# Kernel tuning notes

Hardware: AMD Instinct MI355X
Metric: run time of the kernel (lower is better)

Reference implementation:

```python
import jax, jax.numpy as jnp
import numpy as np

INPUT_SIZE = 64
HIDDEN = 128
BATCH = 256
SEQ = 2048


def setup_inputs() -> dict:
    key = jax.random.key(0)
    k_x, k_w, k_r = jax.random.split(key, 3)
    x = jax.random.normal(k_x, (BATCH, SEQ, INPUT_SIZE), dtype=jnp.float32)
    # Gate order: i, f, o, z (stacked). W: (4H, I), R: (H, 4H), b: (4H,)
    W = jax.random.normal(k_w, (4 * HIDDEN, INPUT_SIZE), dtype=jnp.float32) * (1.0 / np.sqrt(INPUT_SIZE))
    R = jax.random.normal(k_r, (HIDDEN, 4 * HIDDEN), dtype=jnp.float32) * (1.0 / np.sqrt(HIDDEN))
    b = jnp.zeros((4 * HIDDEN,), dtype=jnp.float32)
    return {"x": x, "W": W, "R": R, "b": b}


def _slstm_scan(x, W, R, b):
    B, S, _ = x.shape
    H = R.shape[0]
    # Precompute input projections for all timesteps: (B, S, 4H)
    pre = jnp.einsum('bsi,gi->bsg', x, W) + b
    pre = jnp.swapaxes(pre, 0, 1)  # (S, B, 4H)

    def step(carry, pre_t):
        h, c, n, m = carry
        gates = pre_t + h @ R  # (B, 4H); note: matmul(h, r), NOT r.T (as in source)
        i_t, f_t, o_t, z_t = jnp.split(gates, 4, axis=-1)
        # log(exp(i_tilda)) == i_tilda; log(sigmoid(f_tilda)) stabilized
        log_f = jax.nn.log_sigmoid(f_t)
        m_new = jnp.maximum(log_f + m, i_t)
        i_p = jnp.exp(i_t - m_new)
        f_p = jnp.exp(log_f + m - m_new)
        c_new = f_p * c + i_p * jnp.tanh(z_t)
        n_new = f_p * n + i_p
        h_new = jax.nn.sigmoid(o_t) * jnp.tanh(c_new / n_new)
        return (h_new, c_new, n_new, m_new), h_new

    z = jnp.zeros((B, H), dtype=x.dtype)
    (_h, _c, _n, _m), hs = jax.lax.scan(step, (z, z, z, z), pre)
    return jnp.swapaxes(hs, 0, 1)  # (B, S, H)


def reference(x, W, R, b):
    return _slstm_scan(x, W, R, b)
```

## Files before the change

### kernel.cpp

```cpp
#include <hip/hip_runtime.h>
#include <hip/hip_fp16.h>

#define BATCH 256
#define SEQ   2048
#define ISZ   64
#define HID   128
#define GATES 512
#define KV    192
#define KT    6

typedef _Float16 f16x8 __attribute__((ext_vector_type(8)));
typedef float    f32x4 __attribute__((ext_vector_type(4)));

#if __has_builtin(__builtin_amdgcn_exp2f)
#define EXP2F(v) __builtin_amdgcn_exp2f(v)
#else
#define EXP2F(v) exp2f(v)
#endif
#define RCPF(v) __builtin_amdgcn_rcpf(v)

__global__ __launch_bounds__(512, 2) void slstm_kernel(
    const float* __restrict__ x, const float* __restrict__ W,
    const float* __restrict__ R, const float* __restrict__ bias,
    float* __restrict__ out)
{
    __shared__ __align__(16) _Float16 vh[2][KV];

    const int t    = threadIdx.x;
    const int lane = t & 63;
    const int w    = t >> 6;
    const int c16  = lane & 15;
    const int g    = lane >> 4;
    const int j    = w * 16 + c16;

    const float L2E = 1.4426950408889634f;
    const float sc[4] = {L2E, L2E, L2E, 2.0f * L2E};

    f16x8 bw[4][KT];
#pragma unroll
    for (int q = 0; q < 4; ++q) {
        const int n = q * HID + j;
#pragma unroll
        for (int kt = 0; kt < KT; ++kt) {
            f16x8 v;
#pragma unroll
            for (int e = 0; e < 8; ++e) {
                const int k = kt * 32 + g * 8 + e;
                const float f = (k < ISZ) ? W[n * ISZ + k]
                                          : R[(k - ISZ) * GATES + n];
                v[e] = (_Float16)(f * sc[q]);
            }
            bw[q][kt] = v;
        }
    }

    float bb[4];
#pragma unroll
    for (int q = 0; q < 4; ++q) bb[q] = bias[q * HID + j] * sc[q];

    float C_st = 0.f, N_st = 0.f;

    const float* xb   = x   + (size_t)blockIdx.x * SEQ * ISZ;
    float*       outb = out + (size_t)blockIdx.x * SEQ * HID;

    if (t < HID) vh[0][ISZ + t] = (_Float16)0.f;
    float xreg = 0.f;
    if (t < ISZ) {
        vh[0][t] = (_Float16)xb[t];
        xreg = xb[ISZ + t];
    }
    __syncthreads();

    for (int s = 0; s < SEQ; ++s) {
        const _Float16* vcur = vh[s & 1];
        _Float16*       vnxt = vh[(s + 1) & 1];

        const f16x8* va = (const f16x8*)vcur;
        f16x8 af[KT];
#pragma unroll
        for (int kt = 0; kt < KT; ++kt) af[kt] = va[kt * 4 + g];

        f32x4 acc[4] = {{0.f,0.f,0.f,0.f}, {0.f,0.f,0.f,0.f},
                        {0.f,0.f,0.f,0.f}, {0.f,0.f,0.f,0.f}};
#pragma unroll
        for (int kt = 0; kt < KT; ++kt) {
#pragma unroll
            for (int q = 0; q < 4; ++q)
                acc[q] = __builtin_amdgcn_mfma_f32_16x16x32_f16(
                    af[kt], bw[q][kt], acc[q], 0, 0, 0);
        }

        const float gi = acc[0][0] + bb[0];
        const float gf = acc[1][0] + bb[1];
        const float go = acc[2][0] + bb[2];
        const float gz = acc[3][0] + bb[3];

        const float fp = RCPF(1.f + EXP2F(-gf));
        const float ip = EXP2F(gi);
        const float ez = EXP2F(gz);
        const float tz = 1.f - 2.f * RCPF(ez + 1.f);
        const float so = RCPF(1.f + EXP2F(-go));

        C_st = fp * C_st + ip * tz;
        N_st = fp * N_st + ip;

        const float r  = C_st * RCPF(N_st);
        const float eh = EXP2F(2.8853900817779268f * r);
        const float h  = so * (1.f - 2.f * RCPF(eh + 1.f));

        if (lane < 16) vnxt[ISZ + j] = (_Float16)h;
        if (t < ISZ) {
            vnxt[t] = (_Float16)xreg;
            xreg    = (s + 2 < SEQ) ? xb[(size_t)(s + 2) * ISZ + t] : 0.f;
        }

        asm volatile("s_waitcnt lgkmcnt(0)" ::: "memory");
        __builtin_amdgcn_s_barrier();
        __builtin_amdgcn_sched_barrier(0);

        if (lane < 16) outb[(size_t)s * HID + j] = h;
    }
}

extern "C" void kernel_launch(void* const* d_in, const int* in_sizes, int n_in,
                              void* d_out, int out_size, void* d_ws, size_t ws_size,
                              hipStream_t stream) {
    const float* x = (const float*)d_in[0];
    const float* W = (const float*)d_in[1];
    const float* R = (const float*)d_in[2];
    const float* b = (const float*)d_in[3];
    float* out = (float*)d_out;

    slstm_kernel<<<dim3(BATCH), dim3(512), 0, stream>>>(x, W, R, b, out);
}
```

Before: 1.424 ms.

## Precompute input projections per 16-step window via MFMA, overlapped with recurrence

Instead of pushing x_t through the recurrent MFMA chain every step (K=192), the kernel batches the input projection for 16 timesteps into one MFMA block per window. The result is broadcast per step with shuffles, which shrinks the serial per-step MFMA chain from 6 k-tiles to 4. The next window's x is loaded, staged to LDS and projected at fixed steps inside the current window so the work overlaps the recurrence. This adds shuffles, register pressure and extra LDS staging in exchange for a shorter critical path.

Result: faster. 1.266 ms (-11.1%).

```diff
diff --git a/kernel.cpp b/kernel.cpp
--- a/kernel.cpp
+++ b/kernel.cpp
@@ -6,10 +6,11 @@
 #define ISZ   64
 #define HID   128
 #define GATES 512
-#define KV    192
-#define KT    6
+#define WIN   16
+#define NWIN  (SEQ / WIN)
 
 typedef _Float16 f16x8 __attribute__((ext_vector_type(8)));
+typedef _Float16 f16x4 __attribute__((ext_vector_type(4)));
 typedef float    f32x4 __attribute__((ext_vector_type(4)));
 
 #if __has_builtin(__builtin_amdgcn_exp2f)
@@ -24,7 +25,8 @@
     const float* __restrict__ R, const float* __restrict__ bias,
     float* __restrict__ out)
 {
-    __shared__ __align__(16) _Float16 vh[2][KV];
+    __shared__ __align__(16) _Float16 vh[2][HID];
+    __shared__ __align__(16) _Float16 xblk[2][WIN * ISZ];
 
     const int t    = threadIdx.x;
     const int lane = t & 63;
@@ -36,12 +38,12 @@
     const float L2E = 1.4426950408889634f;
     const float sc[4] = {L2E, L2E, L2E, 2.0f * L2E};
 
-    f16x8 bw[4][KT];
+    f16x8 bw[4][6];
 #pragma unroll
     for (int q = 0; q < 4; ++q) {
         const int n = q * HID + j;
 #pragma unroll
-        for (int kt = 0; kt < KT; ++kt) {
+        for (int kt = 0; kt < 6; ++kt) {
             f16x8 v;
 #pragma unroll
             for (int e = 0; e < 8; ++e) {
@@ -63,62 +65,132 @@
     const float* xb   = x   + (size_t)blockIdx.x * SEQ * ISZ;
     float*       outb = out + (size_t)blockIdx.x * SEQ * HID;
 
-    if (t < HID) vh[0][ISZ + t] = (_Float16)0.f;
-    float xreg = 0.f;
-    if (t < ISZ) {
-        vh[0][t] = (_Float16)xb[t];
-        xreg = xb[ISZ + t];
+    if (t < HID) vh[0][t] = (_Float16)0.f;
+    if (w == 0) {
+#pragma unroll
+        for (int i = 0; i < 4; ++i) {
+            const float4 v = ((const float4*)xb)[i * 64 + lane];
+            f16x4 hv = {(_Float16)v.x, (_Float16)v.y, (_Float16)v.z, (_Float16)v.w};
+            *(f16x4*)((char*)&xblk[0][0] + i * 512 + lane * 8) = hv;
+        }
     }
     __syncthreads();
 
-    for (int s = 0; s < SEQ; ++s) {
-        const _Float16* vcur = vh[s & 1];
-        _Float16*       vnxt = vh[(s + 1) & 1];
-
-        const f16x8* va = (const f16x8*)vcur;
-        f16x8 af[KT];
-#pragma unroll
-        for (int kt = 0; kt < KT; ++kt) af[kt] = va[kt * 4 + g];
-
-        f32x4 acc[4] = {{0.f,0.f,0.f,0.f}, {0.f,0.f,0.f,0.f},
-                        {0.f,0.f,0.f,0.f}, {0.f,0.f,0.f,0.f}};
-#pragma unroll
-        for (int kt = 0; kt < KT; ++kt) {
-#pragma unroll
-            for (int q = 0; q < 4; ++q)
-                acc[q] = __builtin_amdgcn_mfma_f32_16x16x32_f16(
-                    af[kt], bw[q][kt], acc[q], 0, 0, 0);
-        }
-
-        const float gi = acc[0][0] + bb[0];
-        const float gf = acc[1][0] + bb[1];
-        const float go = acc[2][0] + bb[2];
-        const float gz = acc[3][0] + bb[3];
-
-        const float fp = RCPF(1.f + EXP2F(-gf));
-        const float ip = EXP2F(gi);
-        const float ez = EXP2F(gz);
-        const float tz = 1.f - 2.f * RCPF(ez + 1.f);
-        const float so = RCPF(1.f + EXP2F(-go));
-
-        C_st = fp * C_st + ip * tz;
-        N_st = fp * N_st + ip;
-
-        const float r  = C_st * RCPF(N_st);
-        const float eh = EXP2F(2.8853900817779268f * r);
-        const float h  = so * (1.f - 2.f * RCPF(eh + 1.f));
-
-        if (lane < 16) vnxt[ISZ + j] = (_Float16)h;
-        if (t < ISZ) {
-            vnxt[t] = (_Float16)xreg;
-            xreg    = (s + 2 < SEQ) ? xb[(size_t)(s + 2) * ISZ + t] : 0.f;
-        }
-
-        asm volatile("s_waitcnt lgkmcnt(0)" ::: "memory");
-        __builtin_amdgcn_s_barrier();
-        __builtin_amdgcn_sched_barrier(0);
-
-        if (lane < 16) outb[(size_t)s * HID + j] = h;
+    f32x4 pxc[4];
+    {
+        const f16x8* xa = (const f16x8*)&xblk[0][0];
+        const f16x8 xa0 = xa[c16 * 8 + 0 * 4 + g];
+        const f16x8 xa1 = xa[c16 * 8 + 1 * 4 + g];
+#pragma unroll
+        for (int q = 0; q < 4; ++q) {
+            f32x4 a = {0.f, 0.f, 0.f, 0.f};
+            a = __builtin_amdgcn_mfma_f32_16x16x32_f16(xa0, bw[q][0], a, 0, 0, 0);
+            a = __builtin_amdgcn_mfma_f32_16x16x32_f16(xa1, bw[q][1], a, 0, 0, 0);
+            pxc[q] = a;
+        }
+    }
+    f32x4 pxn[4] = {{0.f,0.f,0.f,0.f}, {0.f,0.f,0.f,0.f},
+                    {0.f,0.f,0.f,0.f}, {0.f,0.f,0.f,0.f}};
+
+    for (int win = 0; win < NWIN; ++win) {
+        const bool more = (win + 1 < NWIN);
+        _Float16* xstage = &xblk[(win + 1) & 1][0];
+        float4 xs[4];
+
+#pragma unroll
+        for (int tau = 0; tau < WIN; ++tau) {
+            const int s = win * WIN + tau;
+            const _Float16* hcur = vh[tau & 1];
+            _Float16*       hnxt = vh[(tau + 1) & 1];
+
+            const int src = ((tau & 12) << 2) | c16;
+            const float px0 = __shfl(pxc[0][tau & 3], src);
+            const float px1 = __shfl(pxc[1][tau & 3], src);
+            const float px2 = __shfl(pxc[2][tau & 3], src);
+            const float px3 = __shfl(pxc[3][tau & 3], src);
+
+            const f16x8* ha = (const f16x8*)hcur;
+            f16x8 af0 = ha[0 * 4 + g];
+            f16x8 af1 = ha[1 * 4 + g];
+            f16x8 af2 = ha[2 * 4 + g];
+            f16x8 af3 = ha[3 * 4 + g];
+
+            f32x4 acc[4] = {{0.f,0.f,0.f,0.f}, {0.f,0.f,0.f,0.f},
+                            {0.f,0.f,0.f,0.f}, {0.f,0.f,0.f,0.f}};
+#pragma unroll
+            for (int q = 0; q < 4; ++q)
+                acc[q] = __builtin_amdgcn_mfma_f32_16x16x32_f16(af0, bw[q][2], acc[q], 0, 0, 0);
+#pragma unroll
+            for (int q = 0; q < 4; ++q)
+                acc[q] = __builtin_amdgcn_mfma_f32_16x16x32_f16(af1, bw[q][3], acc[q], 0, 0, 0);
+#pragma unroll
+            for (int q = 0; q < 4; ++q)
+                acc[q] = __builtin_amdgcn_mfma_f32_16x16x32_f16(af2, bw[q][4], acc[q], 0, 0, 0);
+#pragma unroll
+            for (int q = 0; q < 4; ++q)
+                acc[q] = __builtin_amdgcn_mfma_f32_16x16x32_f16(af3, bw[q][5], acc[q], 0, 0, 0);
+
+            if (tau == 1) {
+                if (w == 0 && more) {
+                    const float4* xg = (const float4*)(xb + (size_t)(win + 1) * WIN * ISZ);
+#pragma unroll
+                    for (int i = 0; i < 4; ++i) xs[i] = xg[i * 64 + lane];
+                }
+            }
+            if (tau == 6) {
+                if (w == 0 && more) {
+#pragma unroll
+                    for (int i = 0; i < 4; ++i) {
+                        f16x4 hv = {(_Float16)xs[i].x, (_Float16)xs[i].y,
+                                    (_Float16)xs[i].z, (_Float16)xs[i].w};
+                        *(f16x4*)((char*)xstage + i * 512 + lane * 8) = hv;
+                    }
+                }
+            }
+            if (tau == 10) {
+                if (more) {
+                    const f16x8* xa = (const f16x8*)xstage;
+                    const f16x8 xa0 = xa[c16 * 8 + 0 * 4 + g];
+                    const f16x8 xa1 = xa[c16 * 8 + 1 * 4 + g];
+#pragma unroll
+                    for (int q = 0; q < 4; ++q) {
+                        f32x4 a = {0.f, 0.f, 0.f, 0.f};
+                        a = __builtin_amdgcn_mfma_f32_16x16x32_f16(xa0, bw[q][0], a, 0, 0, 0);
+                        a = __builtin_amdgcn_mfma_f32_16x16x32_f16(xa1, bw[q][1], a, 0, 0, 0);
+                        pxn[q] = a;
+                    }
+                }
+            }
+
+            const float gi = acc[0][0] + px0 + bb[0];
+            const float gf = acc[1][0] + px1 + bb[1];
+            const float go = acc[2][0] + px2 + bb[2];
+            const float gz = acc[3][0] + px3 + bb[3];
+
+            const float fp = RCPF(1.f + EXP2F(-gf));
+            const float ip = EXP2F(gi);
+            const float ez = EXP2F(gz);
+            const float tz = 1.f - 2.f * RCPF(ez + 1.f);
+            const float so = RCPF(1.f + EXP2F(-go));
+
+            C_st = fp * C_st + ip * tz;
+            N_st = fp * N_st + ip;
+
+            const float r  = C_st * RCPF(N_st);
+            const float eh = EXP2F(2.8853900817779268f * r);
+            const float h  = so * (1.f - 2.f * RCPF(eh + 1.f));
+
+            if (lane < 16) hnxt[j] = (_Float16)h;
+
+            asm volatile("s_waitcnt lgkmcnt(0)" ::: "memory");
+            __builtin_amdgcn_s_barrier();
+            __builtin_amdgcn_sched_barrier(0);
+
+            if (lane < 16) outb[(size_t)s * HID + j] = h;
+        }
+
+#pragma unroll
+        for (int q = 0; q < 4; ++q) pxc[q] = pxn[q];
     }
 }
 
```
